# Optimization experiments

Hardware: AMD Instinct MI355X
Metric: run time of the kernel (lower is better)

The kernel has to match this reference:

```python
import jax, jax.numpy as jnp
import numpy as np

D_MODEL = 1024
N_HEADS = 16
HEAD_DIM = D_MODEL // N_HEADS


def setup_inputs() -> dict:
    key = jax.random.key(0)
    ks = jax.random.split(key, 5)
    x = jax.random.normal(ks[0], (4, 2048, D_MODEL), dtype=jnp.float32)
    # qkv Linear: weight [3*d_model, d_model], bias [3*d_model]
    w_qkv = jax.random.normal(ks[1], (3 * D_MODEL, D_MODEL), dtype=jnp.float32) / np.sqrt(D_MODEL)
    b_qkv = jnp.zeros((3 * D_MODEL,), dtype=jnp.float32)
    w_out = jax.random.normal(ks[2], (D_MODEL, D_MODEL), dtype=jnp.float32) / np.sqrt(D_MODEL)
    b_out = jnp.zeros((D_MODEL,), dtype=jnp.float32)
    return {"x": x, "w_qkv": w_qkv, "b_qkv": b_qkv, "w_out": w_out, "b_out": b_out}


def reference(x, w_qkv, b_qkv, w_out, b_out):
    B, T, C = x.shape
    H, Dh = N_HEADS, HEAD_DIM
    qkv = x @ w_qkv.T + b_qkv                      # [B,T,3C]
    qkv = qkv.reshape(B, T, 3, H, Dh)
    q = jnp.transpose(qkv[:, :, 0], (0, 2, 1, 3))  # [B,H,T,Dh]
    k = jnp.transpose(qkv[:, :, 1], (0, 2, 1, 3))
    v = jnpp_transpose = jnp.transpose(qkv[:, :, 2], (0, 2, 1, 3))
    scale = 1.0 / np.sqrt(Dh).astype(np.float32)
    att = jnp.einsum('bhqd,bhkd->bhqk', q, k) * scale
    causal = jnp.tril(jnp.ones((T, T), dtype=bool))
    att = jnp.where(causal[None, None], att, -jnp.inf)
    att = jax.nn.softmax(att, axis=-1)
    head_out = jnp.einsum('bhqk,bhkd->bhqd', att, v)  # [B,H,T,Dh]
    out = jnp.transpose(head_out, (0, 2, 1, 3)).reshape(B, T, C)
    return out @ w_out.T + b_out
```

## Files before the change

kernel.cpp:

```cpp
#include <hip/hip_runtime.h>
#include <hip/hip_bf16.h>


#define D_MODEL 1024
#define N_HEADS 16
#define HEAD_DIM 64
#define SEQ 2048
#define BATCH 4

typedef __attribute__((ext_vector_type(8))) short bf16x8;
typedef __attribute__((ext_vector_type(4))) float f32x4;
typedef unsigned int uint;

__device__ __forceinline__ short f2bf(float f) {
    union { float f; uint i; } c; c.f = f;
    uint x = c.i;
    x += 0x7fffu + ((x >> 16) & 1u);
    return (short)(x >> 16);
}
__device__ __forceinline__ uint pack2(float a, float b) {
    return (uint)(unsigned short)f2bf(a) | ((uint)(unsigned short)f2bf(b) << 16);
}
__device__ __forceinline__ uint asu(float f) { union { float f; uint i; } c; c.f = f; return c.i; }
__device__ __forceinline__ uint packtr(float lo, float hi) {
    return (asu(lo) >> 16) | (asu(hi) & 0xffff0000u);
}

__device__ __forceinline__ void glds16(const void* g, void* l) {
    __builtin_amdgcn_global_load_lds(
        (const __attribute__((address_space(1))) uint*)g,
        (__attribute__((address_space(3))) uint*)l, 16, 0, 0);
}

__global__ __launch_bounds__(256) void cvt3_bf16(const float* __restrict__ s0,
                                                 const float* __restrict__ s1,
                                                 const float* __restrict__ s2,
                                                 short* __restrict__ dst,
                                                 int n0, int n01) {
    int i = blockIdx.x * 256 + threadIdx.x;
    const float* src;
    int off;
    if (i < n0)       { src = s0; off = i; }
    else if (i < n01) { src = s1; off = i - n0; }
    else              { src = s2; off = i - n01; }
    float4 f = *(const float4*)(src + (size_t)off * 4);
    uint2 o; o.x = pack2(f.x, f.y); o.y = pack2(f.z, f.w);
    *(uint2*)(dst + (size_t)i * 4) = o;
}

template <int MODE>
__global__ __launch_bounds__(256, 2) void gemm_bt(
    const short* __restrict__ A, const short* __restrict__ B,
    const float* __restrict__ bias, float* __restrict__ Cp,
    int M, int N, int K,
    short* __restrict__ qp, short* __restrict__ kp, short* __restrict__ vp)
{
    __shared__ short As[128][32];
    __shared__ short Bs[128][32];
    const int tid = threadIdx.x;
    const int wave = tid >> 6, lane = tid & 63;
    const int quad = lane >> 4, l16 = lane & 15;
    const int wm = (wave >> 1) * 64, wn = (wave & 1) * 64;
    const int rowBase = blockIdx.y * 128;
    const int colBase = blockIdx.x * 128;

    const short* gA = A + (size_t)(rowBase + wave * 32 + (lane >> 2)) * K + (lane & 3) * 8;
    const short* gB = B + (size_t)(colBase + wave * 32 + (lane >> 2)) * K + (lane & 3) * 8;
    void* lA0 = &As[wave * 32][0];
    void* lA1 = &As[wave * 32 + 16][0];
    void* lB0 = &Bs[wave * 32][0];
    void* lB1 = &Bs[wave * 32 + 16][0];

    f32x4 acc[4][4] = {};

    for (int k0 = 0; k0 < K; k0 += 32) {
        __syncthreads();
        glds16(gA + k0, lA0);
        glds16(gA + (size_t)16 * K + k0, lA1);
        glds16(gB + k0, lB0);
        glds16(gB + (size_t)16 * K + k0, lB1);
        __syncthreads();
        bf16x8 af[4], bfr[4];
#pragma unroll
        for (int i = 0; i < 4; ++i)
            af[i] = *(const bf16x8*)&As[wm + i * 16 + l16][quad * 8];
#pragma unroll
        for (int j = 0; j < 4; ++j)
            bfr[j] = *(const bf16x8*)&Bs[wn + j * 16 + l16][quad * 8];
#pragma unroll
        for (int i = 0; i < 4; ++i)
#pragma unroll
            for (int j = 0; j < 4; ++j)
                acc[i][j] = __builtin_amdgcn_mfma_f32_16x16x32_bf16(af[i], bfr[j], acc[i][j], 0, 0, 0);
    }

#pragma unroll
    for (int i = 0; i < 4; ++i) {
#pragma unroll
        for (int j = 0; j < 4; ++j) {
#pragma unroll
            for (int r = 0; r < 4; ++r) {
                int row = rowBase + wm + i * 16 + quad * 4 + r;
                int col = colBase + wn + j * 16 + l16;
                float v = acc[i][j][r] + bias[col];
                if (MODE == 0) {
                    Cp[(size_t)row * N + col] = v;
                } else {
                    int which = col >> 10;
                    int h = (col >> 6) & 15;
                    int d = col & 63;
                    int b = row >> 11;
                    int t = row & 2047;
                    short* dst = (which == 0) ? qp : (which == 1) ? kp : vp;
                    dst[((((size_t)b * N_HEADS + h) * SEQ) + t) * HEAD_DIM + d] = f2bf(v);
                }
            }
        }
    }
}

__global__ __launch_bounds__(256, 2) void attn_fwd(
    const short* __restrict__ Q, const short* __restrict__ K,
    const short* __restrict__ V, short* __restrict__ O)
{
    __shared__ short Ks[64][72];
    __shared__ short Vt[64][72];
    __shared__ short Ps[128][72];
    const int tid = threadIdx.x;
    const int wave = tid >> 6, lane = tid & 63;
    const int quad = lane >> 4, l16 = lane & 15;
    const int bh = blockIdx.x;
    const int b = bh >> 4, h = bh & 15;
    const int qt = gridDim.y - 1 - blockIdx.y;
    const int qbase = qt * 128;
    const short* Qh = Q + (size_t)bh * SEQ * HEAD_DIM;
    const short* Kh = K + (size_t)bh * SEQ * HEAD_DIM;
    const short* Vh = V + (size_t)bh * SEQ * HEAD_DIM;

    bf16x8 qf[2][2];
#pragma unroll
    for (int m = 0; m < 2; ++m)
#pragma unroll
        for (int st = 0; st < 2; ++st)
            qf[m][st] = *(const bf16x8*)(Qh + (size_t)(qbase + wave * 32 + m * 16 + l16) * HEAD_DIM + st * 32 + quad * 8);

    f32x4 o[2][4] = {};
    f32x4 osum[2] = {};
    const float C1 = 0.125f * 1.44269504f;
    const float C2 = 14.4269504f;

    bf16x8 onesf;
#pragma unroll
    for (int e = 0; e < 8; ++e) onesf[e] = (short)0x3F80;

    const int kr = tid >> 2, kc = (tid & 3) * 16;
    const int vk = (tid & 31) * 2, vd = (tid >> 5) * 8;
    const int subw = qbase + wave * 32;

    const int ntiles = 2 * qt + 2;
    int4 kv0 = *(const int4*)(Kh + (size_t)kr * HEAD_DIM + kc);
    int4 kv1 = *(const int4*)(Kh + (size_t)kr * HEAD_DIM + kc + 8);
    int4 vv0 = *(const int4*)(Vh + (size_t)vk * HEAD_DIM + vd);
    int4 vv1 = *(const int4*)(Vh + (size_t)(vk + 1) * HEAD_DIM + vd);

    for (int j = 0; j < ntiles; ++j) {
        const int kb = j * 64;
        __syncthreads();
        *(int4*)&Ks[kr][kc] = kv0;
        *(int4*)&Ks[kr][kc + 8] = kv1;
        {
            const short* va = (const short*)&vv0;
            const short* vb = (const short*)&vv1;
#pragma unroll
            for (int e = 0; e < 8; ++e)
                *(uint*)&Vt[vd + e][vk] =
                    (uint)(unsigned short)va[e] | ((uint)(unsigned short)vb[e] << 16);
        }
        __syncthreads();

        {
            const int kbn = (j + 1 < ntiles) ? kb + 64 : kb;
            kv0 = *(const int4*)(Kh + (size_t)(kbn + kr) * HEAD_DIM + kc);
            kv1 = *(const int4*)(Kh + (size_t)(kbn + kr) * HEAD_DIM + kc + 8);
            vv0 = *(const int4*)(Vh + (size_t)(kbn + vk) * HEAD_DIM + vd);
            vv1 = *(const int4*)(Vh + (size_t)(kbn + vk + 1) * HEAD_DIM + vd);
        }

        if (kb > subw + 31) continue;

        f32x4 s[2][4];
#pragma unroll
        for (int kt = 0; kt < 4; ++kt) {
            bf16x8 kf0 = *(const bf16x8*)&Ks[kt * 16 + l16][quad * 8];
            bf16x8 kf1 = *(const bf16x8*)&Ks[kt * 16 + l16][32 + quad * 8];
#pragma unroll
            for (int m = 0; m < 2; ++m) {
                f32x4 t = {0.f, 0.f, 0.f, 0.f};
                t = __builtin_amdgcn_mfma_f32_16x16x32_bf16(kf0, qf[m][0], t, 0, 0, 0);
                t = __builtin_amdgcn_mfma_f32_16x16x32_bf16(kf1, qf[m][1], t, 0, 0, 0);
                s[m][kt] = t;
            }
        }
#pragma unroll
        for (int m = 0; m < 2; ++m) {
            const int sub = subw + m * 16;
            const int qrow = sub + l16;
            const bool needmask = (kb + 63 > sub);
            const int prow = wave * 32 + m * 16 + l16;
#pragma unroll
            for (int kt = 0; kt < 4; ++kt) {
                float p[4];
#pragma unroll
                for (int r = 0; r < 4; ++r) {
                    float a = __builtin_fmaf(s[m][kt][r], C1, -C2);
                    if (needmask && (kb + kt * 16 + quad * 4 + r > qrow)) a = -1e30f;
                    p[r] = __builtin_exp2f(a);
                }
                uint2 u; u.x = packtr(p[0], p[1]); u.y = packtr(p[2], p[3]);
                *(uint2*)&Ps[prow][kt * 16 + quad * 4] = u;
            }
        }
#pragma unroll
        for (int st = 0; st < 2; ++st) {
            bf16x8 pf0 = *(const bf16x8*)&Ps[wave * 32 + l16][st * 32 + quad * 8];
            bf16x8 pf1 = *(const bf16x8*)&Ps[wave * 32 + 16 + l16][st * 32 + quad * 8];
            osum[0] = __builtin_amdgcn_mfma_f32_16x16x32_bf16(pf0, onesf, osum[0], 0, 0, 0);
            osum[1] = __builtin_amdgcn_mfma_f32_16x16x32_bf16(pf1, onesf, osum[1], 0, 0, 0);
#pragma unroll
            for (int dt = 0; dt < 4; ++dt) {
                bf16x8 vf = *(const bf16x8*)&Vt[dt * 16 + l16][st * 32 + quad * 8];
                o[0][dt] = __builtin_amdgcn_mfma_f32_16x16x32_bf16(pf0, vf, o[0][dt], 0, 0, 0);
                o[1][dt] = __builtin_amdgcn_mfma_f32_16x16x32_bf16(pf1, vf, o[1][dt], 0, 0, 0);
            }
        }
    }

#pragma unroll
    for (int m = 0; m < 2; ++m) {
#pragma unroll
        for (int r = 0; r < 4; ++r) {
            float inv = 1.f / osum[m][r];
            int t = qbase + wave * 32 + m * 16 + quad * 4 + r;
            size_t base = ((size_t)b * SEQ + t) * D_MODEL + h * HEAD_DIM;
#pragma unroll
            for (int dt = 0; dt < 4; ++dt)
                O[base + dt * 16 + l16] = f2bf(o[m][dt][r] * inv);
        }
    }
}

extern "C" void kernel_launch(void* const* d_in, const int* in_sizes, int n_in,
                              void* d_out, int out_size, void* d_ws, size_t ws_size,
                              hipStream_t stream)
{
    const float* x     = (const float*)d_in[0];
    const float* w_qkv = (const float*)d_in[1];
    const float* b_qkv = (const float*)d_in[2];
    const float* w_out = (const float*)d_in[3];
    const float* b_out = (const float*)d_in[4];
    float* out = (float*)d_out;

    const int NX = BATCH * SEQ * D_MODEL;
    const int NWQ = 3 * D_MODEL * D_MODEL;
    const int NWO = D_MODEL * D_MODEL;
    const size_t HE = (size_t)BATCH * N_HEADS * SEQ * HEAD_DIM;

    short* xb    = (short*)d_ws;
    short* wqkvb = xb + NX;
    short* woutb = wqkvb + NWQ;
    short* qp    = woutb + NWO;
    short* kp    = qp + HE;
    short* vp    = kp + HE;
    short* ho    = xb;

    const int M = BATCH * SEQ;

    cvt3_bf16<<<(NX + NWQ + NWO) / 1024, 256, 0, stream>>>(
        x, w_qkv, w_out, xb, NX / 4, (NX + NWQ) / 4);

    gemm_bt<1><<<dim3(3 * D_MODEL / 128, M / 128), 256, 0, stream>>>(
        xb, wqkvb, b_qkv, nullptr, M, 3 * D_MODEL, D_MODEL, qp, kp, vp);

    attn_fwd<<<dim3(BATCH * N_HEADS, SEQ / 128), 256, 0, stream>>>(qp, kp, vp, ho);

    gemm_bt<0><<<dim3(D_MODEL / 128, M / 128), 256, 0, stream>>>(
        ho, woutb, b_out, out, M, D_MODEL, D_MODEL, nullptr, nullptr, nullptr);
}
```

Before: 259.5 us.

## Pair causal query tiles per block to balance attention work

Each attention block now handles two query tiles, one from the long end (15-y) and one from the short end (y), which halves the grid and gives every block the same causal workload. The softmax masking is split per 16-key subtile into fully-masked (skip the exp), unmasked, and diagonal cases, with the row base made wave-uniform through readfirstlane. The V transpose now packs pairs with byte-perm instructions. The grid drops to 512 blocks, which may reduce occupancy and latency hiding on a GPU with many CUs.

```diff
diff --git a/kernel.cpp b/kernel.cpp
--- a/kernel.cpp
+++ b/kernel.cpp
@@ -131,21 +131,10 @@
     const int quad = lane >> 4, l16 = lane & 15;
     const int bh = blockIdx.x;
     const int b = bh >> 4, h = bh & 15;
-    const int qt = gridDim.y - 1 - blockIdx.y;
-    const int qbase = qt * 128;
     const short* Qh = Q + (size_t)bh * SEQ * HEAD_DIM;
     const short* Kh = K + (size_t)bh * SEQ * HEAD_DIM;
     const short* Vh = V + (size_t)bh * SEQ * HEAD_DIM;
 
-    bf16x8 qf[2][2];
-#pragma unroll
-    for (int m = 0; m < 2; ++m)
-#pragma unroll
-        for (int st = 0; st < 2; ++st)
-            qf[m][st] = *(const bf16x8*)(Qh + (size_t)(qbase + wave * 32 + m * 16 + l16) * HEAD_DIM + st * 32 + quad * 8);
-
-    f32x4 o[2][4] = {};
-    f32x4 osum[2] = {};
     const float C1 = 0.125f * 1.44269504f;
     const float C2 = 14.4269504f;
 
@@ -155,96 +144,127 @@
 
     const int kr = tid >> 2, kc = (tid & 3) * 16;
     const int vk = (tid & 31) * 2, vd = (tid >> 5) * 8;
-    const int subw = qbase + wave * 32;
-
-    const int ntiles = 2 * qt + 2;
-    int4 kv0 = *(const int4*)(Kh + (size_t)kr * HEAD_DIM + kc);
-    int4 kv1 = *(const int4*)(Kh + (size_t)kr * HEAD_DIM + kc + 8);
-    int4 vv0 = *(const int4*)(Vh + (size_t)vk * HEAD_DIM + vd);
-    int4 vv1 = *(const int4*)(Vh + (size_t)(vk + 1) * HEAD_DIM + vd);
-
-    for (int j = 0; j < ntiles; ++j) {
-        const int kb = j * 64;
-        __syncthreads();
-        *(int4*)&Ks[kr][kc] = kv0;
-        *(int4*)&Ks[kr][kc + 8] = kv1;
-        {
-            const short* va = (const short*)&vv0;
-            const short* vb = (const short*)&vv1;
-#pragma unroll
-            for (int e = 0; e < 8; ++e)
-                *(uint*)&Vt[vd + e][vk] =
-                    (uint)(unsigned short)va[e] | ((uint)(unsigned short)vb[e] << 16);
+
+    for (int pass = 0; pass < 2; ++pass) {
+        const int qt = pass == 0 ? (15 - (int)blockIdx.y) : (int)blockIdx.y;
+        const int qbase = qt * 128;
+
+        bf16x8 qf[2][2];
+#pragma unroll
+        for (int m = 0; m < 2; ++m)
+#pragma unroll
+            for (int st = 0; st < 2; ++st)
+                qf[m][st] = *(const bf16x8*)(Qh + (size_t)(qbase + wave * 32 + m * 16 + l16) * HEAD_DIM + st * 32 + quad * 8);
+
+        f32x4 o[2][4] = {};
+        f32x4 osum[2] = {};
+
+        const int subw = qbase + wave * 32;
+        const int subS = __builtin_amdgcn_readfirstlane(subw);
+
+        const int ntiles = 2 * qt + 2;
+        int4 kv0 = *(const int4*)(Kh + (size_t)kr * HEAD_DIM + kc);
+        int4 kv1 = *(const int4*)(Kh + (size_t)kr * HEAD_DIM + kc + 8);
+        int4 vv0 = *(const int4*)(Vh + (size_t)vk * HEAD_DIM + vd);
+        int4 vv1 = *(const int4*)(Vh + (size_t)(vk + 1) * HEAD_DIM + vd);
+
+        for (int j = 0; j < ntiles; ++j) {
+            const int kb = j * 64;
+            __syncthreads();
+            *(int4*)&Ks[kr][kc] = kv0;
+            *(int4*)&Ks[kr][kc + 8] = kv1;
+            {
+                const uint* pa = (const uint*)&vv0;
+                const uint* pb = (const uint*)&vv1;
+#pragma unroll
+                for (int e = 0; e < 4; ++e) {
+                    uint lo = __builtin_amdgcn_perm(pb[e], pa[e], 0x05040100u);
+                    uint hi = __builtin_amdgcn_perm(pb[e], pa[e], 0x07060302u);
+                    *(uint*)&Vt[vd + 2 * e][vk] = lo;
+                    *(uint*)&Vt[vd + 2 * e + 1][vk] = hi;
+                }
+            }
+            __syncthreads();
+
+            {
+                const int kbn = (j + 1 < ntiles) ? kb + 64 : kb;
+                kv0 = *(const int4*)(Kh + (size_t)(kbn + kr) * HEAD_DIM + kc);
+                kv1 = *(const int4*)(Kh + (size_t)(kbn + kr) * HEAD_DIM + kc + 8);
+                vv0 = *(const int4*)(Vh + (size_t)(kbn + vk) * HEAD_DIM + vd);
+                vv1 = *(const int4*)(Vh + (size_t)(kbn + vk + 1) * HEAD_DIM + vd);
+            }
+
+            if (kb > subS + 31) continue;
+
+            f32x4 s[2][4];
+#pragma unroll
+            for (int kt = 0; kt < 4; ++kt) {
+                bf16x8 kf0 = *(const bf16x8*)&Ks[kt * 16 + l16][quad * 8];
+                bf16x8 kf1 = *(const bf16x8*)&Ks[kt * 16 + l16][32 + quad * 8];
+#pragma unroll
+                for (int m = 0; m < 2; ++m) {
+                    f32x4 t = {0.f, 0.f, 0.f, 0.f};
+                    t = __builtin_amdgcn_mfma_f32_16x16x32_bf16(kf0, qf[m][0], t, 0, 0, 0);
+                    t = __builtin_amdgcn_mfma_f32_16x16x32_bf16(kf1, qf[m][1], t, 0, 0, 0);
+                    s[m][kt] = t;
+                }
+            }
+#pragma unroll
+            for (int m = 0; m < 2; ++m) {
+                const int sub = subS + m * 16;
+                const int qrow = sub + l16;
+                const int prow = wave * 32 + m * 16 + l16;
+#pragma unroll
+                for (int kt = 0; kt < 4; ++kt) {
+                    const int kbkt = kb + kt * 16;
+                    uint2 u;
+                    if (kbkt > sub + 15) {
+                        u.x = 0u; u.y = 0u;
+                    } else if (kbkt + 15 <= sub) {
+                        float p[4];
+#pragma unroll
+                        for (int r = 0; r < 4; ++r)
+                            p[r] = __builtin_exp2f(__builtin_fmaf(s[m][kt][r], C1, -C2));
+                        u.x = packtr(p[0], p[1]); u.y = packtr(p[2], p[3]);
+                    } else {
+                        float p[4];
+#pragma unroll
+                        for (int r = 0; r < 4; ++r) {
+                            float a = __builtin_fmaf(s[m][kt][r], C1, -C2);
+                            if (kbkt + quad * 4 + r > qrow) a = -1e30f;
+                            p[r] = __builtin_exp2f(a);
+                        }
+                        u.x = packtr(p[0], p[1]); u.y = packtr(p[2], p[3]);
+                    }
+                    *(uint2*)&Ps[prow][kt * 16 + quad * 4] = u;
+                }
+            }
+#pragma unroll
+            for (int st = 0; st < 2; ++st) {
+                bf16x8 pf0 = *(const bf16x8*)&Ps[wave * 32 + l16][st * 32 + quad * 8];
+                bf16x8 pf1 = *(const bf16x8*)&Ps[wave * 32 + 16 + l16][st * 32 + quad * 8];
+                osum[0] = __builtin_amdgcn_mfma_f32_16x16x32_bf16(pf0, onesf, osum[0], 0, 0, 0);
+                osum[1] = __builtin_amdgcn_mfma_f32_16x16x32_bf16(pf1, onesf, osum[1], 0, 0, 0);
+#pragma unroll
+                for (int dt = 0; dt < 4; ++dt) {
+                    bf16x8 vf = *(const bf16x8*)&Vt[dt * 16 + l16][st * 32 + quad * 8];
+                    o[0][dt] = __builtin_amdgcn_mfma_f32_16x16x32_bf16(pf0, vf, o[0][dt], 0, 0, 0);
+                    o[1][dt] = __builtin_amdgcn_mfma_f32_16x16x32_bf16(pf1, vf, o[1][dt], 0, 0, 0);
+                }
+            }
         }
-        __syncthreads();
-
-        {
-            const int kbn = (j + 1 < ntiles) ? kb + 64 : kb;
-            kv0 = *(const int4*)(Kh + (size_t)(kbn + kr) * HEAD_DIM + kc);
-            kv1 = *(const int4*)(Kh + (size_t)(kbn + kr) * HEAD_DIM + kc + 8);
-            vv0 = *(const int4*)(Vh + (size_t)(kbn + vk) * HEAD_DIM + vd);
-            vv1 = *(const int4*)(Vh + (size_t)(kbn + vk + 1) * HEAD_DIM + vd);
-        }
-
-        if (kb > subw + 31) continue;
-
-        f32x4 s[2][4];
-#pragma unroll
-        for (int kt = 0; kt < 4; ++kt) {
-            bf16x8 kf0 = *(const bf16x8*)&Ks[kt * 16 + l16][quad * 8];
-            bf16x8 kf1 = *(const bf16x8*)&Ks[kt * 16 + l16][32 + quad * 8];
-#pragma unroll
-            for (int m = 0; m < 2; ++m) {
-                f32x4 t = {0.f, 0.f, 0.f, 0.f};
-                t = __builtin_amdgcn_mfma_f32_16x16x32_bf16(kf0, qf[m][0], t, 0, 0, 0);
-                t = __builtin_amdgcn_mfma_f32_16x16x32_bf16(kf1, qf[m][1], t, 0, 0, 0);
-                s[m][kt] = t;
-            }
-        }
+
 #pragma unroll
         for (int m = 0; m < 2; ++m) {
-            const int sub = subw + m * 16;
-            const int qrow = sub + l16;
-            const bool needmask = (kb + 63 > sub);
-            const int prow = wave * 32 + m * 16 + l16;
-#pragma unroll
-            for (int kt = 0; kt < 4; ++kt) {
-                float p[4];
-#pragma unroll
-                for (int r = 0; r < 4; ++r) {
-                    float a = __builtin_fmaf(s[m][kt][r], C1, -C2);
-                    if (needmask && (kb + kt * 16 + quad * 4 + r > qrow)) a = -1e30f;
-                    p[r] = __builtin_exp2f(a);
-                }
-                uint2 u; u.x = packtr(p[0], p[1]); u.y = packtr(p[2], p[3]);
-                *(uint2*)&Ps[prow][kt * 16 + quad * 4] = u;
-            }
-        }
-#pragma unroll
-        for (int st = 0; st < 2; ++st) {
-            bf16x8 pf0 = *(const bf16x8*)&Ps[wave * 32 + l16][st * 32 + quad * 8];
-            bf16x8 pf1 = *(const bf16x8*)&Ps[wave * 32 + 16 + l16][st * 32 + quad * 8];
-            osum[0] = __builtin_amdgcn_mfma_f32_16x16x32_bf16(pf0, onesf, osum[0], 0, 0, 0);
-            osum[1] = __builtin_amdgcn_mfma_f32_16x16x32_bf16(pf1, onesf, osum[1], 0, 0, 0);
-#pragma unroll
-            for (int dt = 0; dt < 4; ++dt) {
-                bf16x8 vf = *(const bf16x8*)&Vt[dt * 16 + l16][st * 32 + quad * 8];
-                o[0][dt] = __builtin_amdgcn_mfma_f32_16x16x32_bf16(pf0, vf, o[0][dt], 0, 0, 0);
-                o[1][dt] = __builtin_amdgcn_mfma_f32_16x16x32_bf16(pf1, vf, o[1][dt], 0, 0, 0);
-            }
-        }
-    }
-
-#pragma unroll
-    for (int m = 0; m < 2; ++m) {
-#pragma unroll
-        for (int r = 0; r < 4; ++r) {
-            float inv = 1.f / osum[m][r];
-            int t = qbase + wave * 32 + m * 16 + quad * 4 + r;
-            size_t base = ((size_t)b * SEQ + t) * D_MODEL + h * HEAD_DIM;
-#pragma unroll
-            for (int dt = 0; dt < 4; ++dt)
-                O[base + dt * 16 + l16] = f2bf(o[m][dt][r] * inv);
+#pragma unroll
+            for (int r = 0; r < 4; ++r) {
+                float inv = 1.f / osum[m][r];
+                int t = qbase + wave * 32 + m * 16 + quad * 4 + r;
+                size_t base = ((size_t)b * SEQ + t) * D_MODEL + h * HEAD_DIM;
+#pragma unroll
+                for (int dt = 0; dt < 4; ++dt)
+                    O[base + dt * 16 + l16] = f2bf(o[m][dt][r] * inv);
+            }
         }
     }
 }
@@ -281,7 +301,7 @@
     gemm_bt<1><<<dim3(3 * D_MODEL / 128, M / 128), 256, 0, stream>>>(
         xb, wqkvb, b_qkv, nullptr, M, 3 * D_MODEL, D_MODEL, qp, kp, vp);
 
-    attn_fwd<<<dim3(BATCH * N_HEADS, SEQ / 128), 256, 0, stream>>>(qp, kp, vp, ho);
+    attn_fwd<<<dim3(BATCH * N_HEADS, SEQ / 256), 256, 0, stream>>>(qp, kp, vp, ho);
 
     gemm_bt<0><<<dim3(D_MODEL / 128, M / 128), 256, 0, stream>>>(
         ho, woutb, b_out, out, M, D_MODEL, D_MODEL, nullptr, nullptr, nullptr);
```

New measurement: 265.3 us. 1.02x slower.
